# Optimization experiments

Hardware: AMD Instinct MI355X
Metric: run time of the kernel (lower is better)

The kernel has to match this reference:

```python
import jax, jax.numpy as jnp
import numpy as np

N_FREQ = 128
N_SPACE = 3
DIS_DIM = 2 * N_FREQ * N_SPACE  # 768


def sin_emb(x):
    # x: [E, 3] -> [E, 768]; frequencies = 2*pi*arange(n_freq) as in DiffCSP SinusoidsEmbedding
    freq = 2.0 * jnp.pi * jnp.arange(N_FREQ, dtype=x.dtype)
    e = (x[..., None] * freq).reshape(x.shape[0], N_SPACE * N_FREQ)
    return jnp.concatenate([jnp.sin(e), jnp.cos(e)], axis=-1)


def layer_norm(x, g, b, eps=1e-5):
    m = jnp.mean(x, axis=-1, keepdims=True)
    v = jnp.var(x, axis=-1, keepdims=True)
    return (x - m) * jax.lax.rsqrt(v + eps) * g + b


def setup_inputs() -> dict:
    key = jax.random.key(0)
    ks = jax.random.split(key, 16)
    N, E, B, H = 10000, 200000, 50, 512
    E_IN = 2 * H + DIS_DIM + 6  # 1798
    s = 0.02
    return {
        "node_features": jax.random.normal(ks[0], (N, H), jnp.float32),
        "lattices": jax.random.normal(ks[1], (B, 6), jnp.float32),
        "edge_index": jax.random.randint(ks[2], (2, E), 0, N),
        "edge2graph": jax.random.randint(ks[3], (E,), 0, B),
        "frac_diff": jax.random.uniform(ks[4], (E, 3), jnp.float32),
        "num_atoms": jax.random.randint(ks[5], (B,), 1, 200),
        "ln_gamma": jnp.ones((H,), jnp.float32),
        "ln_beta": jnp.zeros((H,), jnp.float32),
        "W_e1": jax.random.normal(ks[6], (E_IN, H), jnp.float32) * s,
        "b_e1": jnp.zeros((H,), jnp.float32),
        "W_e2": jax.random.normal(ks[7], (H, H), jnp.float32) * s,
        "b_e2": jnp.zeros((H,), jnp.float32),
        "W_n1": jax.random.normal(ks[8], (2 * H, H), jnp.float32) * s,
        "b_n1": jnp.zeros((H,), jnp.float32),
        "W_n2": jax.random.normal(ks[9], (H, H), jnp.float32) * s,
        "b_n2": jnp.zeros((H,), jnp.float32),
    }


def reference(node_features, lattices, edge_index, edge2graph, frac_diff, num_atoms,
              ln_gamma, ln_beta, W_e1, b_e1, W_e2, b_e2, W_n1, b_n1, W_n2, b_n2):
    N = node_features.shape[0]
    # pre-LN (ln=True): residual uses raw input
    h = layer_norm(node_features, ln_gamma, ln_beta)
    # edge model: gather + concat + 2-layer MLP with SiLU
    hi = h[edge_index[0]]
    hj = h[edge_index[1]]
    fd = sin_emb(frac_diff)
    lat_e = lattices.reshape(lattices.shape[0], -1)[edge2graph]
    e_in = jnp.concatenate([hi, hj, lat_e, fd], axis=1)  # [E, 1798]
    e = jax.nn.silu(e_in @ W_e1 + b_e1)
    e = jax.nn.silu(e @ W_e2 + b_e2)
    # node model: scatter-mean over edge source + 2-layer MLP
    agg = jax.ops.segment_sum(e, edge_index[0], num_segments=N)
    cnt = jax.ops.segment_sum(jnp.ones((e.shape[0],), e.dtype), edge_index[0], num_segments=N)
    agg = agg / jnp.maximum(cnt, 1.0)[:, None]
    n_in = jnp.concatenate([h, agg], axis=1)  # [N, 1024]
    o = jax.nn.silu(n_in @ W_n1 + b_n1)
    o = jax.nn.silu(o @ W_n2 + b_n2)
    return node_features + o
```

## Files before the change

kernel.cpp:

```cpp
#include <hip/hip_runtime.h>
#include <hip/hip_bf16.h>


#include <type_traits>

typedef __attribute__((ext_vector_type(8))) short bfrag;
typedef __attribute__((ext_vector_type(4))) float ffrag;

#define DEVI __device__ __forceinline__

constexpr int N_NODES = 10000;
constexpr int N_EDGES = 200000;
constexpr int HD      = 512;
constexpr int NT      = HD / 16;
constexpr int SLABW   = 520;
constexpr int FSW     = 260;
constexpr int KSTR    = NT * 64 * 8;

DEVI float silu_f(float v) {
    return v * __builtin_amdgcn_rcpf(1.0f + __expf(-v));
}

DEVI ushort f2bf(float f) {
    unsigned u = __float_as_uint(f);
    unsigned r = (u + 0x7fffu + ((u >> 16) & 1u)) >> 16;
    return (ushort)r;
}
DEVI float bf2f(ushort v) { return __uint_as_float((unsigned)v << 16); }

DEVI int cperm(int col) {
    return (col & ~63) | ((col & 15) << 2) | ((col >> 4) & 3);
}

__global__ void wswz_kernel(const float* __restrict__ W, ushort* __restrict__ dst,
                            int Kp, int mode) {
    int fid = blockIdx.x * blockDim.x + threadIdx.x;
    int total = (Kp / 32) * NT * 64;
    if (fid >= total) return;
    int l  = fid & 63;
    int nn = (fid >> 6) & 31;
    int kk = fid >> 11;
    int col = nn * 16 + (l & 15);
    int kb  = kk * 32 + (l >> 4) * 8;
    union { ushort u16[8]; uint4 u4; } v;
    for (int j = 0; j < 8; ++j) {
        int krow = kb + j;
        int src;
        if (mode == 3) {
            int d = krow >> 8, rm = krow & 255, k = rm >> 1;
            src = ((rm & 1) ? 1414 : 1030) + d * 128 + k;
        } else if (mode == 1) {
            src = (krow & ~63) | ((krow & 3) << 4) | ((krow >> 2) & 15);
        } else if (mode == 2) {
            src = (krow < 512) ? krow
                : ((krow & ~63) | ((krow & 3) << 4) | ((krow >> 2) & 15));
        } else {
            src = krow;
        }
        v.u16[j] = f2bf(W[(size_t)src * HD + col]);
    }
    *(uint4*)(dst + (size_t)fid * 8) = v.u4;
}

__global__ void ln_kernel(const float* __restrict__ x, const float* __restrict__ g,
                          const float* __restrict__ b, ushort* __restrict__ h) {
    __shared__ float wred[8];
    __shared__ float mb[2];
    int row = blockIdx.x;
    int t = threadIdx.x;
    const float* xr = x + (size_t)row * HD;
    float2 xv = *(const float2*)(xr + 2 * t);
    float s = xv.x + xv.y, qq = xv.x * xv.x + xv.y * xv.y;
    for (int o = 32; o; o >>= 1) { s += __shfl_down(s, o); qq += __shfl_down(qq, o); }
    int w = t >> 6, l = t & 63;
    if (l == 0) { wred[w] = s; wred[w + 4] = qq; }
    __syncthreads();
    if (t == 0) {
        float S = wred[0] + wred[1] + wred[2] + wred[3];
        float Q = wred[4] + wred[5] + wred[6] + wred[7];
        float m = S * (1.0f / HD);
        float v = Q * (1.0f / HD) - m * m;
        mb[0] = m; mb[1] = rsqrtf(v + 1e-5f);
    }
    __syncthreads();
    float m = mb[0], rs = mb[1];
    float2 gv = *(const float2*)(g + 2 * t);
    float2 bv = *(const float2*)(b + 2 * t);
    __hip_bfloat162 o2 = __float22bfloat162_rn(
        float2{(xv.x - m) * rs * gv.x + bv.x, (xv.y - m) * rs * gv.y + bv.y});
    *(__hip_bfloat162*)(h + (size_t)row * HD + 2 * t) = o2;
}

__global__ void latb_kernel(const float* __restrict__ latt, const float* __restrict__ W_e1,
                            const float* __restrict__ b1, float* __restrict__ LATBp) {
    int g = blockIdx.x;
    int t = threadIdx.x;
    float a = b1[t];
    for (int c = 0; c < 6; ++c)
        a += latt[g * 6 + c] * W_e1[(size_t)(1024 + c) * HD + t];
    LATBp[(size_t)g * HD + cperm(t)] = a;
}

__global__ void zero_kernel(int* __restrict__ c32, float4* __restrict__ agg4) {
    int i = blockIdx.x * 256 + threadIdx.x;
    if (i < N_NODES) c32[i] = 0;
    agg4[i] = float4{0.f, 0.f, 0.f, 0.f};
}

__global__ void hist_kernel(const int* __restrict__ eidx, int* __restrict__ cnt32) {
    int e = blockIdx.x * 256 + threadIdx.x;
    if (e < N_EDGES) atomicAdd(&cnt32[eidx[e]], 1);
}

__global__ void scan_kernel(const int* __restrict__ cnt32, int* __restrict__ row_ptr,
                            int* __restrict__ cursor) {
    __shared__ int buf[1024];
    int t = threadIdx.x;
    int base = t * 10;
    int loc[10]; int s = 0;
    for (int i = 0; i < 10; ++i) {
        int idx = base + i;
        int v = (idx < N_NODES) ? cnt32[idx] : 0;
        loc[i] = s; s += v;
    }
    buf[t] = s; __syncthreads();
    for (int off = 1; off < 1024; off <<= 1) {
        int v = 0; if (t >= off) v = buf[t - off];
        __syncthreads();
        buf[t] += v; __syncthreads();
    }
    int excl = buf[t] - s;
    for (int i = 0; i < 10; ++i) {
        int idx = base + i;
        if (idx < N_NODES) { int p = excl + loc[i]; row_ptr[idx] = p; cursor[idx] = p; }
    }
    if (t == 0) row_ptr[N_NODES] = N_EDGES;
}

__global__ void csr_fill(const int* __restrict__ eidx, int* __restrict__ cursor,
                         int* __restrict__ ebuf) {
    int e = blockIdx.x * 256 + threadIdx.x;
    if (e >= N_EDGES) return;
    int pos = atomicAdd(&cursor[eidx[e]], 1);
    ebuf[pos] = e;
}

__global__ void aggdiv_kernel(const float* __restrict__ agg, const int* __restrict__ rp,
                              ushort* __restrict__ aggb) {
    int i = blockIdx.x * 256 + threadIdx.x;
    int row = i >> 8;
    int deg = rp[row + 1] - rp[row];
    float rc = __builtin_amdgcn_rcpf((float)max(deg, 1));
    float2 v = *(const float2*)(agg + (size_t)i * 2);
    *(__hip_bfloat162*)(aggb + (size_t)i * 2) =
        __float22bfloat162_rn(float2{v.x * rc, v.y * rc});
}

__global__ void sentinel_kernel(float* o, int n) {
    int i = blockIdx.x * 256 + threadIdx.x;
    if (i < n) o[i] = 123456789.0f;
}

template <int KTN, int MT>
DEVI void kloop_rot(ffrag (&acc)[MT][4], const ushort* sl, const ushort* bp0,
                    int ml, int q) {
    bfrag b_[4];
    const ushort* bp = bp0;
    #pragma unroll
    for (int n = 0; n < 4; ++n) b_[n] = *(const bfrag*)(bp + n * 512);
    #pragma unroll
    for (int p = 0; p < KTN; ++p) {
        bfrag a_[MT];
        #pragma unroll
        for (int m = 0; m < MT; ++m)
            a_[m] = *(const bfrag*)&sl[(16 * m + ml) * SLABW + p * 32 + q * 8];
        const ushort* bpn = bp + KSTR;
        #pragma unroll
        for (int n = 0; n < 4; ++n) {
            #pragma unroll
            for (int m = 0; m < MT; ++m)
                acc[m][n] = __builtin_amdgcn_mfma_f32_16x16x32_bf16(a_[m], b_[n], acc[m][n], 0, 0, 0);
            if (p + 1 < KTN) b_[n] = *(const bfrag*)(bpn + n * 512);
        }
        bp = bpn;
    }
}

__global__ __launch_bounds__(512, 4) void hab_gemm(
    const ushort* __restrict__ h, const ushort* __restrict__ w1a_s,
    const ushort* __restrict__ w1b_s, ushort* __restrict__ HAp,
    ushort* __restrict__ HBp) {

    __shared__ __align__(16) ushort slab[32 * SLABW];
    const int t = threadIdx.x;
    const int w = t >> 6;
    const int l = t & 63;
    const int q = l >> 4;
    const int ml = l & 15;
    const int rowbase = blockIdx.x * 32;
    const ushort* Bswz = blockIdx.y ? w1b_s : w1a_s;
    ushort* out = blockIdx.y ? HBp : HAp;

    for (int j = 0; j < 4; ++j) {
        int rr = w * 4 + j;
        int row = rowbase + rr;
        if (row >= N_NODES) row = N_NODES - 1;
        *(uint4*)&slab[rr * SLABW + l * 8] =
            *(const uint4*)(h + (size_t)row * HD + l * 8);
    }
    __syncthreads();

    ffrag acc[2][4];
    for (int m = 0; m < 2; ++m)
        for (int n = 0; n < 4; ++n)
            acc[m][n] = (ffrag){0.f, 0.f, 0.f, 0.f};

    kloop_rot<16, 2>(acc, slab, Bswz + ((size_t)(w << 2) * 64 + l) * 8, ml, q);

    for (int m = 0; m < 2; ++m)
        for (int rr = 0; rr < 4; ++rr) {
            int grow = rowbase + 16 * m + 4 * q + rr;
            if (grow < N_NODES) {
                union { __hip_bfloat162 h2[2]; ushort4 u4; } pk;
                pk.h2[0] = __float22bfloat162_rn(float2{acc[m][0][rr], acc[m][1][rr]});
                pk.h2[1] = __float22bfloat162_rn(float2{acc[m][2][rr], acc[m][3][rr]});
                *(ushort4*)(out + (size_t)grow * HD + w * 64 + ml * 4) = pk.u4;
            }
        }
}

__global__ __launch_bounds__(512, 4) void edge_mlp(
    const ushort* __restrict__ HAp,   const ushort* __restrict__ HBp,
    const float* __restrict__ LATBp,  const ushort* __restrict__ w1c,
    const ushort* __restrict__ w2s,   const float* __restrict__ b2,
    float* __restrict__ agg,
    const int* __restrict__ edge_index, const int* __restrict__ e2g,
    const float* __restrict__ frac_diff, const int* __restrict__ ebuf) {

    __shared__ __align__(16) ushort slab[64 * SLABW];
    __shared__ int   ssrc[64];
    __shared__ int   sdst[64];
    __shared__ int   sgrp[64];
    __shared__ float sfd[64 * 3];

    const int t = threadIdx.x;
    const int w = t >> 6;
    const int l = t & 63;
    const int q = l >> 4;
    const int ml = l & 15;
    const int rowbase = blockIdx.x * 64;

    if (t < 64) {
        int eid = ebuf[rowbase + t];
        ssrc[t] = edge_index[eid];
        sdst[t] = edge_index[N_EDGES + eid];
        sgrp[t] = e2g[eid];
        for (int c = 0; c < 3; ++c) sfd[t * 3 + c] = frac_diff[(size_t)eid * 3 + c];
    }
    __syncthreads();

    ffrag acc[4][4];
    {
        const int cb = w * 64 + ml * 4;
        for (int m = 0; m < 4; ++m)
            for (int rr = 0; rr < 4; ++rr) {
                int rowl = 16 * m + 4 * q + rr;
                ushort4 a4 = *(const ushort4*)(HAp + (size_t)ssrc[rowl] * HD + cb);
                ushort4 h4 = *(const ushort4*)(HBp + (size_t)sdst[rowl] * HD + cb);
                float4  l4 = *(const float4*)(LATBp + (size_t)sgrp[rowl] * HD + cb);
                acc[m][0][rr] = bf2f(a4.x) + bf2f(h4.x) + l4.x;
                acc[m][1][rr] = bf2f(a4.y) + bf2f(h4.y) + l4.y;
                acc[m][2][rr] = bf2f(a4.z) + bf2f(h4.z) + l4.z;
                acc[m][3][rr] = bf2f(a4.w) + bf2f(h4.w) + l4.w;
            }
    }

    const int r  = t >> 3;
    const int c0 = (t & 7) * 4;
    float fd3[3] = { sfd[r * 3 + 0], sfd[r * 3 + 1], sfd[r * 3 + 2] };

    auto stage = [&](int phase) {
        float s = 0.f, c = 0.f, sx = 0.f, cx = 0.f, s16 = 0.f, c16 = 0.f;
        int dcur = -1;
        #pragma unroll
        for (int i = 0; i < 12; ++i) {
            int cc = c0 + 32 * i;
            int cp = phase * 384 + cc;
            int d = cp >> 8;
            if (d != dcur) {
                dcur = d;
                float x = fd3[d];
                float rx = __builtin_amdgcn_fractf(x);
                sx  = __builtin_amdgcn_sinf(rx);
                cx  = __builtin_amdgcn_cosf(rx);
                float r16 = __builtin_amdgcn_fractf(16.0f * x);
                s16 = __builtin_amdgcn_sinf(r16);
                c16 = __builtin_amdgcn_cosf(r16);
                int k0 = (cp & 255) >> 1;
                float r0 = __builtin_amdgcn_fractf((float)k0 * x);
                s = __builtin_amdgcn_sinf(r0);
                c = __builtin_amdgcn_cosf(r0);
            } else {
                float ns = s * c16 + c * s16;
                float nc = c * c16 - s * s16;
                s = ns; c = nc;
            }
            float s1 = s * cx + c * sx;
            float c1 = c * cx - s * sx;
            union { __hip_bfloat162 h2[2]; ushort4 u4; } pk;
            pk.h2[0] = __float22bfloat162_rn(float2{s, c});
            pk.h2[1] = __float22bfloat162_rn(float2{s1, c1});
            *(ushort4*)&slab[r * SLABW + cc] = pk.u4;
        }
    };

    const ushort* bpw1 = w1c + ((size_t)(w << 2) * 64 + l) * 8;
    const ushort* bpw2 = w2s + ((size_t)(w << 2) * 64 + l) * 8;

    stage(0);
    __syncthreads();
    kloop_rot<12, 4>(acc, slab, bpw1, ml, q);
    __syncthreads();
    stage(1);
    __syncthreads();
    kloop_rot<12, 4>(acc, slab, bpw1 + (size_t)12 * KSTR, ml, q);
    __syncthreads();

    for (int m = 0; m < 4; ++m)
        for (int rr = 0; rr < 4; ++rr) {
            int rowl = 16 * m + 4 * q + rr;
            union { __hip_bfloat162 h2[2]; ushort4 u4; } pk;
            pk.h2[0] = __float22bfloat162_rn(
                float2{silu_f(acc[m][0][rr]), silu_f(acc[m][1][rr])});
            pk.h2[1] = __float22bfloat162_rn(
                float2{silu_f(acc[m][2][rr]), silu_f(acc[m][3][rr])});
            *(ushort4*)&slab[rowl * SLABW + w * 64 + ml * 4] = pk.u4;
        }
    for (int m = 0; m < 4; ++m)
        for (int n = 0; n < 4; ++n)
            acc[m][n] = (ffrag){0.f, 0.f, 0.f, 0.f};
    __syncthreads();

    kloop_rot<16, 4>(acc, slab, bpw2, ml, q);

    float* fs = (float*)slab;
    float bv0 = b2[w * 64 + 0 * 16 + ml];
    float bv1 = b2[w * 64 + 1 * 16 + ml];
    float bv2 = b2[w * 64 + 2 * 16 + ml];
    float bv3 = b2[w * 64 + 3 * 16 + ml];
    for (int hh = 0; hh < 2; ++hh) {
        __syncthreads();
        if ((w >> 2) == hh) {
            int lcb = w * 64 + ml * 4 - hh * 256;
            for (int m = 0; m < 4; ++m)
                for (int rr = 0; rr < 4; ++rr) {
                    int rowl = 16 * m + 4 * q + rr;
                    float4 v = float4{silu_f(acc[m][0][rr] + bv0),
                                      silu_f(acc[m][1][rr] + bv1),
                                      silu_f(acc[m][2][rr] + bv2),
                                      silu_f(acc[m][3][rr] + bv3)};
                    *(float4*)&fs[rowl * FSW + lcb] = v;
                }
        }
        __syncthreads();
        {
            int col = t & 255;
            int r0 = (t >> 8) * 32;
            int cur = ssrc[r0];
            float run = 0.f;
            for (int j = 0; j < 32; ++j) {
                int rr2 = r0 + j;
                int nd = ssrc[rr2];
                if (nd != cur) {
                    unsafeAtomicAdd(&agg[(size_t)cur * HD + hh * 256 + col], run);
                    run = 0.f; cur = nd;
                }
                run += fs[rr2 * FSW + col];
            }
            unsafeAtomicAdd(&agg[(size_t)cur * HD + hh * 256 + col], run);
        }
    }
}

__global__ __launch_bounds__(512, 4) void node_mlp(
    const ushort* __restrict__ h,     const ushort* __restrict__ aggb,
    const ushort* __restrict__ wn1s,  const ushort* __restrict__ wn2s,
    const float* __restrict__ b1,     const float* __restrict__ b2,
    const float* __restrict__ nf,     float* __restrict__ out) {

    __shared__ __align__(16) ushort slab[32 * SLABW];

    const int t = threadIdx.x;
    const int w = t >> 6;
    const int l = t & 63;
    const int q = l >> 4;
    const int ml = l & 15;
    const int rowbase = blockIdx.x * 32;

    ffrag acc[2][4];
    for (int m = 0; m < 2; ++m)
        for (int n = 0; n < 4; ++n)
            acc[m][n] = (ffrag){0.f, 0.f, 0.f, 0.f};

    auto load_rows = [&](const ushort* base) {
        for (int j = 0; j < 4; ++j) {
            int rr = w * 4 + j;
            int row = rowbase + rr;
            if (row >= N_NODES) row = N_NODES - 1;
            *(uint4*)&slab[rr * SLABW + l * 8] =
                *(const uint4*)(base + (size_t)row * HD + l * 8);
        }
    };
    const ushort* bp1 = wn1s + ((size_t)(w << 2) * 64 + l) * 8;
    const ushort* bp2 = wn2s + ((size_t)(w << 2) * 64 + l) * 8;

    load_rows(h);                        __syncthreads();
    kloop_rot<16, 2>(acc, slab, bp1, ml, q);
    __syncthreads();
    load_rows(aggb);                     __syncthreads();
    kloop_rot<16, 2>(acc, slab, bp1 + (size_t)16 * KSTR, ml, q);
    __syncthreads();

    {
        float bv[4];
        for (int n = 0; n < 4; ++n) bv[n] = b1[w * 64 + n * 16 + ml];
        for (int m = 0; m < 2; ++m)
            for (int rr = 0; rr < 4; ++rr) {
                int rowl = 16 * m + 4 * q + rr;
                union { __hip_bfloat162 h2[2]; ushort4 u4; } pk;
                pk.h2[0] = __float22bfloat162_rn(
                    float2{silu_f(acc[m][0][rr] + bv[0]), silu_f(acc[m][1][rr] + bv[1])});
                pk.h2[1] = __float22bfloat162_rn(
                    float2{silu_f(acc[m][2][rr] + bv[2]), silu_f(acc[m][3][rr] + bv[3])});
                *(ushort4*)&slab[rowl * SLABW + w * 64 + ml * 4] = pk.u4;
            }
    }
    for (int m = 0; m < 2; ++m)
        for (int n = 0; n < 4; ++n)
            acc[m][n] = (ffrag){0.f, 0.f, 0.f, 0.f};
    __syncthreads();

    kloop_rot<16, 2>(acc, slab, bp2, ml, q);

    for (int n = 0; n < 4; ++n) {
        int cg = w * 64 + n * 16 + ml;
        float bv = b2[cg];
        for (int m = 0; m < 2; ++m)
            for (int rr = 0; rr < 4; ++rr) {
                int rowl = 16 * m + 4 * q + rr;
                int row = rowbase + rowl;
                if (row < N_NODES) {
                    float v = silu_f(acc[m][n][rr] + bv);
                    out[(size_t)row * HD + cg] = nf[(size_t)row * HD + cg] + v;
                }
            }
    }
}

extern "C" void kernel_launch(void* const* d_in, const int* in_sizes, int n_in,
                              void* d_out, int out_size, void* d_ws, size_t ws_size,
                              hipStream_t stream) {
    const float* nf      = (const float*)d_in[0];
    const float* latt    = (const float*)d_in[1];
    const int*   eidx    = (const int*)d_in[2];
    const int*   e2g     = (const int*)d_in[3];
    const float* fd      = (const float*)d_in[4];
    const float* ln_g    = (const float*)d_in[6];
    const float* ln_b    = (const float*)d_in[7];
    const float* W_e1    = (const float*)d_in[8];
    const float* b_e1    = (const float*)d_in[9];
    const float* W_e2    = (const float*)d_in[10];
    const float* b_e2    = (const float*)d_in[11];
    const float* W_n1    = (const float*)d_in[12];
    const float* b_n1    = (const float*)d_in[13];
    const float* W_n2    = (const float*)d_in[14];
    const float* b_n2    = (const float*)d_in[15];
    float* out = (float*)d_out;

    auto al = [](size_t x) { return (x + 511) & ~(size_t)511; };
    size_t off_h    = 0;                         size_t sz_h    = (size_t)N_NODES * HD * 2;
    size_t off_w1a  = al(off_h + sz_h);          size_t sz_w1a  = (size_t)HD * HD * 2;
    size_t off_w1b  = al(off_w1a + sz_w1a);      size_t sz_w1b  = (size_t)HD * HD * 2;
    size_t off_w1c  = al(off_w1b + sz_w1b);      size_t sz_w1c  = (size_t)768 * HD * 2;
    size_t off_w2   = al(off_w1c + sz_w1c);      size_t sz_w2   = (size_t)HD * HD * 2;
    size_t off_wn1  = al(off_w2 + sz_w2);        size_t sz_wn1  = (size_t)2 * HD * HD * 2;
    size_t off_wn2  = al(off_wn1 + sz_wn1);      size_t sz_wn2  = (size_t)HD * HD * 2;
    size_t off_ha   = al(off_wn2 + sz_wn2);      size_t sz_ha   = (size_t)N_NODES * HD * 2;
    size_t off_hb   = al(off_ha + sz_ha);        size_t sz_hb   = (size_t)N_NODES * HD * 2;
    size_t off_lb   = al(off_hb + sz_hb);        size_t sz_lb   = (size_t)50 * HD * 4;
    size_t off_agb  = al(off_lb + sz_lb);        size_t sz_agb  = (size_t)N_NODES * HD * 2;
    size_t off_c32  = al(off_agb + sz_agb);      size_t sz_c32  = (size_t)N_NODES * 4;
    size_t off_cur  = al(off_c32 + sz_c32);      size_t sz_cur  = (size_t)N_NODES * 4;
    size_t off_rp   = al(off_cur + sz_cur);      size_t sz_rp   = (size_t)(N_NODES + 1) * 4;
    size_t off_ebuf = al(off_rp + sz_rp);        size_t sz_ebuf = (size_t)N_EDGES * 4;
    size_t off_agg  = al(off_ebuf + sz_ebuf);    size_t sz_agg  = (size_t)N_NODES * HD * 4;
    size_t need     = off_agg + sz_agg;

    if (ws_size < need) {
        sentinel_kernel<<<(out_size + 255) / 256, 256, 0, stream>>>(out, out_size);
        return;
    }

    char* ws = (char*)d_ws;
    ushort* h     = (ushort*)(ws + off_h);
    ushort* w1a_s = (ushort*)(ws + off_w1a);
    ushort* w1b_s = (ushort*)(ws + off_w1b);
    ushort* w1c_s = (ushort*)(ws + off_w1c);
    ushort* w2s   = (ushort*)(ws + off_w2);
    ushort* wn1s  = (ushort*)(ws + off_wn1);
    ushort* wn2s  = (ushort*)(ws + off_wn2);
    ushort* HAp   = (ushort*)(ws + off_ha);
    ushort* HBp   = (ushort*)(ws + off_hb);
    float*  LATBp = (float*)(ws + off_lb);
    ushort* aggb  = (ushort*)(ws + off_agb);
    int*    c32   = (int*)(ws + off_c32);
    int*    cur   = (int*)(ws + off_cur);
    int*    rp    = (int*)(ws + off_rp);
    int*    ebuf  = (int*)(ws + off_ebuf);
    float*  agg   = (float*)(ws + off_agg);

    zero_kernel<<<(N_NODES * HD / 4) / 256, 256, 0, stream>>>(c32, (float4*)agg);
    wswz_kernel<<<(HD / 32) * NT * 64 / 256, 256, 0, stream>>>(W_e1, w1a_s, HD, 0);
    wswz_kernel<<<(HD / 32) * NT * 64 / 256, 256, 0, stream>>>(W_e1 + (size_t)HD * HD, w1b_s, HD, 0);
    wswz_kernel<<<(768 / 32) * NT * 64 / 256, 256, 0, stream>>>(W_e1, w1c_s, 768, 3);
    wswz_kernel<<<(HD / 32) * NT * 64 / 256, 256, 0, stream>>>(W_e2, w2s, HD, 1);
    wswz_kernel<<<(2 * HD / 32) * NT * 64 / 256, 256, 0, stream>>>(W_n1, wn1s, 2 * HD, 2);
    wswz_kernel<<<(HD / 32) * NT * 64 / 256, 256, 0, stream>>>(W_n2, wn2s, HD, 1);
    latb_kernel<<<50, 512, 0, stream>>>(latt, W_e1, b_e1, LATBp);

    hist_kernel<<<(N_EDGES + 255) / 256, 256, 0, stream>>>(eidx, c32);
    scan_kernel<<<1, 1024, 0, stream>>>(c32, rp, cur);
    csr_fill<<<(N_EDGES + 255) / 256, 256, 0, stream>>>(eidx, cur, ebuf);

    ln_kernel<<<N_NODES, 256, 0, stream>>>(nf, ln_g, ln_b, h);
    hab_gemm<<<dim3(313, 2), 512, 0, stream>>>(h, w1a_s, w1b_s, HAp, HBp);

    edge_mlp<<<N_EDGES / 64, 512, 0, stream>>>(
        HAp, HBp, LATBp, w1c_s, w2s, b_e2, agg, eidx, e2g, fd, ebuf);

    aggdiv_kernel<<<(N_NODES * HD / 2) / 256, 256, 0, stream>>>(agg, rp, aggb);

    int nblocks = (N_NODES + 31) / 32;
    node_mlp<<<nblocks, 512, 0, stream>>>(h, aggb, wn1s, wn2s, b_n1, b_n2, nf, out);
}
```

Baseline: 538.0 us.

## Interleave sinusoid embedding generation with MFMA k-loop using double-buffered slab halves

New measurement: 541.2 us. No clear change (+0.6%).

```diff
diff --git a/kernel.cpp b/kernel.cpp
--- a/kernel.cpp
+++ b/kernel.cpp
@@ -186,6 +186,32 @@
     }
 }
 
+template <int KTN, int MT, typename F>
+DEVI void kloop_fill(ffrag (&acc)[MT][4], const ushort* sl, const ushort* bp0,
+                     int ml, int q, F&& fill) {
+    bfrag b_[4];
+    const ushort* bp = bp0;
+    #pragma unroll
+    for (int n = 0; n < 4; ++n) b_[n] = *(const bfrag*)(bp + n * 512);
+    #pragma unroll
+    for (int p = 0; p < KTN; ++p) {
+        bfrag a_[MT];
+        #pragma unroll
+        for (int m = 0; m < MT; ++m)
+            a_[m] = *(const bfrag*)&sl[(16 * m + ml) * SLABW + p * 32 + q * 8];
+        const ushort* bpn = bp + KSTR;
+        #pragma unroll
+        for (int n = 0; n < 4; ++n) {
+            #pragma unroll
+            for (int m = 0; m < MT; ++m)
+                acc[m][n] = __builtin_amdgcn_mfma_f32_16x16x32_bf16(a_[m], b_[n], acc[m][n], 0, 0, 0);
+            if (p + 1 < KTN) b_[n] = *(const bfrag*)(bpn + n * 512);
+        }
+        fill(p);
+        bp = bpn;
+    }
+}
+
 __global__ __launch_bounds__(512, 4) void hab_gemm(
     const ushort* __restrict__ h, const ushort* __restrict__ w1a_s,
     const ushort* __restrict__ w1b_s, ushort* __restrict__ HAp,
@@ -277,53 +303,38 @@
 
     const int r  = t >> 3;
     const int c0 = (t & 7) * 4;
-    float fd3[3] = { sfd[r * 3 + 0], sfd[r * 3 + 1], sfd[r * 3 + 2] };
-
-    auto stage = [&](int phase) {
-        float s = 0.f, c = 0.f, sx = 0.f, cx = 0.f, s16 = 0.f, c16 = 0.f;
-        int dcur = -1;
-        #pragma unroll
-        for (int i = 0; i < 12; ++i) {
-            int cc = c0 + 32 * i;
-            int cp = phase * 384 + cc;
-            int d = cp >> 8;
-            if (d != dcur) {
-                dcur = d;
-                float x = fd3[d];
-                float rx = __builtin_amdgcn_fractf(x);
-                sx  = __builtin_amdgcn_sinf(rx);
-                cx  = __builtin_amdgcn_cosf(rx);
-                float r16 = __builtin_amdgcn_fractf(16.0f * x);
-                s16 = __builtin_amdgcn_sinf(r16);
-                c16 = __builtin_amdgcn_cosf(r16);
-                int k0 = (cp & 255) >> 1;
-                float r0 = __builtin_amdgcn_fractf((float)k0 * x);
-                s = __builtin_amdgcn_sinf(r0);
-                c = __builtin_amdgcn_cosf(r0);
-            } else {
-                float ns = s * c16 + c * s16;
-                float nc = c * c16 - s * s16;
-                s = ns; c = nc;
-            }
-            float s1 = s * cx + c * sx;
-            float c1 = c * cx - s * sx;
-            union { __hip_bfloat162 h2[2]; ushort4 u4; } pk;
-            pk.h2[0] = __float22bfloat162_rn(float2{s, c});
-            pk.h2[1] = __float22bfloat162_rn(float2{s1, c1});
-            *(ushort4*)&slab[r * SLABW + cc] = pk.u4;
-        }
+
+    auto stage_item = [&](int qq, int i) {
+        int cc = (qq & 1) * 192 + c0 + 32 * i;
+        int cp = qq * 192 + c0 + 32 * i;
+        int d = cp >> 8;
+        float x = sfd[r * 3 + d];
+        float f0 = (float)((cp & 255) >> 1) * x;
+        float r0 = __builtin_amdgcn_fractf(f0);
+        float r1 = __builtin_amdgcn_fractf(f0 + x);
+        union { __hip_bfloat162 h2[2]; ushort4 u4; } pk;
+        pk.h2[0] = __float22bfloat162_rn(float2{__builtin_amdgcn_sinf(r0),
+                                                __builtin_amdgcn_cosf(r0)});
+        pk.h2[1] = __float22bfloat162_rn(float2{__builtin_amdgcn_sinf(r1),
+                                                __builtin_amdgcn_cosf(r1)});
+        *(ushort4*)&slab[r * SLABW + cc] = pk.u4;
     };
 
     const ushort* bpw1 = w1c + ((size_t)(w << 2) * 64 + l) * 8;
     const ushort* bpw2 = w2s + ((size_t)(w << 2) * 64 + l) * 8;
 
-    stage(0);
-    __syncthreads();
-    kloop_rot<12, 4>(acc, slab, bpw1, ml, q);
-    __syncthreads();
-    stage(1);
-    __syncthreads();
-    kloop_rot<12, 4>(acc, slab, bpw1 + (size_t)12 * KSTR, ml, q);
+    for (int i = 0; i < 6; ++i) stage_item(0, i);
+    __syncthreads();
+    kloop_fill<6, 4>(acc, slab, bpw1, ml, q,
+                     [&](int p) { stage_item(1, p); });
+    __syncthreads();
+    kloop_fill<6, 4>(acc, slab + 192, bpw1 + (size_t)6 * KSTR, ml, q,
+                     [&](int p) { stage_item(2, p); });
+    __syncthreads();
+    kloop_fill<6, 4>(acc, slab, bpw1 + (size_t)12 * KSTR, ml, q,
+                     [&](int p) { stage_item(3, p); });
+    __syncthreads();
+    kloop_rot<6, 4>(acc, slab + 192, bpw1 + (size_t)18 * KSTR, ml, q);
     __syncthreads();
 
     for (int m = 0; m < 4; ++m)
```
